# Kernel optimization log

Hardware: AMD Instinct MI355X
Metric: run time of the kernel (lower is better)

## Reference

```python
import jax, jax.numpy as jnp
import numpy as np

SCALE = 0.25  # LoRA alpha / rank


def setup_inputs() -> dict:
    N, K, E, H, D, R = 1024, 2, 16, 1024, 2048, 16
    key = jax.random.key(0)
    ks = jax.random.split(key, 9)
    hidden_states = jax.random.normal(ks[0], (N, D), jnp.float32)
    topk_weights = jax.random.uniform(ks[1], (N, K), jnp.float32)
    topk_weights = topk_weights / topk_weights.sum(-1, keepdims=True)
    topk_ids = jax.random.randint(ks[2], (N, K), 0, E, jnp.int32)
    w_up = jax.random.normal(ks[3], (E, 2 * H, D), jnp.float32) * 0.02
    w_down = jax.random.normal(ks[4], (E, D, H), jnp.float32) * 0.02
    up_a = jax.random.normal(ks[5], (E, R, D), jnp.float32) * 0.02
    up_b = jax.random.normal(ks[6], (E, 2 * H, R), jnp.float32) * 0.02
    down_a = jax.random.normal(ks[7], (E, R, H), jnp.float32) * 0.02
    down_b = jax.random.normal(ks[8], (E, D, R), jnp.float32) * 0.02
    return {
        'hidden_states': hidden_states,
        'topk_weights': topk_weights,
        'topk_ids': topk_ids,
        'w_up': w_up,
        'w_down': w_down,
        'up_a': up_a,
        'up_b': up_b,
        'down_a': down_a,
        'down_b': down_b,
    }


def reference(hidden_states, topk_weights, topk_ids, w_up, w_down, up_a, up_b, down_a, down_b):
    H = w_down.shape[2]  # hidden_size
    # Up projection: dense per-expert GEMM, then gather the selected expert per (token, k).
    up_dense = jnp.einsum('nd,eod->neo', hidden_states, w_up)          # [N, E, 2H]
    up = jnp.take_along_axis(up_dense, topk_ids[:, :, None], axis=1)   # [N, K, 2H]
    # LoRA on up-proj: out[:, k] += (x @ A_e.T @ B_e.T) * scale
    t = jnp.einsum('nd,nkrd->nkr', hidden_states, up_a[topk_ids])      # [N, K, R]
    up = up + SCALE * jnp.einsum('nkr,nkor->nko', t, up_b[topk_ids])   # [N, K, 2H]
    # fused_gelu_and_mul: gelu(first half) * second half (erf gelu)
    act = jax.nn.gelu(up[..., :H], approximate=False) * up[..., H:]    # [N, K, H]
    # Down projection with routed-weight multiply.
    down_dense = jnp.einsum('nkh,edh->nked', act, w_down)              # [N, K, E, D]
    down = jnp.take_along_axis(down_dense, topk_ids[:, :, None, None], axis=2)[:, :, 0, :]  # [N, K, D]
    # LoRA on down-proj (topk_weights applied to lora path too, matching _apply_moe_lora)
    t2 = jnp.einsum('nkh,nkrh->nkr', act, down_a[topk_ids])            # [N, K, R]
    ldown = jnp.einsum('nkr,nkdr->nkd', t2, down_b[topk_ids])          # [N, K, D]
    down = (down + SCALE * ldown) * topk_weights[:, :, None]
    # moe_sum: reduce over top_k
    return down.sum(axis=1)                                            # [N, D]
```

## Files before the change

kernel.cpp:

```cpp
#include <hip/hip_runtime.h>
#include <math.h>

#define N_TOK 1024
#define TOPK  2
#define NEXP  16
#define HID   1024
#define DIM   2048
#define RANK  16
#define NPAIR (N_TOK * TOPK)
#define MOE_SCALE 0.25f
#define MAXTILES 31

typedef __attribute__((ext_vector_type(8))) short short8;
typedef __attribute__((ext_vector_type(4))) float floatx4;

static __device__ __forceinline__ unsigned short f2bf(float f) {
    union { float f; unsigned int u; } v; v.f = f;
    unsigned int u = v.u;
    u += 0x7fffu + ((u >> 16) & 1u);
    return (unsigned short)(u >> 16);
}

static __device__ __forceinline__ short8 cvt8(float4 a, float4 b) {
    short8 o;
    o[0] = (short)f2bf(a.x); o[1] = (short)f2bf(a.y);
    o[2] = (short)f2bf(a.z); o[3] = (short)f2bf(a.w);
    o[4] = (short)f2bf(b.x); o[5] = (short)f2bf(b.y);
    o[6] = (short)f2bf(b.z); o[7] = (short)f2bf(b.w);
    return o;
}

#define XG_T16_STRIDE   (64 * 64 * 8)
#define ACT_T16_STRIDE  (32 * 64 * 8)

__global__ void k_routing(const int* __restrict__ ids,
                          int* __restrict__ offs,
                          int* __restrict__ sorted,
                          int* __restrict__ tlist,
                          int* __restrict__ tcount) {
    __shared__ int s_cnt[NEXP];
    __shared__ int s_off[NEXP + 1];
    int tid = threadIdx.x;
    if (tid < NEXP) s_cnt[tid] = 0;
    __syncthreads();
    for (int p = tid; p < NPAIR; p += blockDim.x) atomicAdd(&s_cnt[ids[p]], 1);
    __syncthreads();
    if (tid == 0) {
        int acc = 0;
        for (int e = 0; e < NEXP; ++e) { s_off[e] = acc; acc += s_cnt[e]; }
        s_off[NEXP] = acc;
        int t = 0;
        for (int e = 0; e < NEXP; ++e) {
            int c = s_off[e + 1] - s_off[e];
            for (int m = 0; m * 128 < c; ++m) tlist[t++] = (e << 8) | m;
        }
        *tcount = t;
    }
    __syncthreads();
    if (tid <= NEXP) offs[tid] = s_off[tid];
    if (tid < NEXP) s_cnt[tid] = s_off[tid];
    __syncthreads();
    for (int p = tid; p < NPAIR; p += blockDim.x) {
        int e = ids[p];
        int slot = atomicAdd(&s_cnt[e], 1);
        sorted[slot] = p;
    }
}

__global__ __launch_bounds__(256) void k_prep(
        const float* __restrict__ x, const int* __restrict__ offs,
        const int* __restrict__ sorted, const int* __restrict__ tlist,
        const int* __restrict__ tcount, unsigned short* __restrict__ xg) {
    int wt = blockIdx.x;
    if (wt >= *tcount) return;
    int code = tlist[wt];
    int e = code >> 8, mt = code & 255;
    int off = offs[e], cnt = offs[e + 1] - off;
    int tid = threadIdx.x, lane = tid & 63, wv = tid >> 6;
    int C = blockIdx.y * 4 + wv;
    int r16 = lane & 15, lq = lane >> 4;
#pragma unroll
    for (int st = 0; st < 8; ++st) {
        int g = mt * 128 + st * 16 + r16; if (g >= cnt) g = cnt - 1;
        int tok = sorted[off + g] >> 1;
        const float* src = x + (size_t)tok * DIM + C * 32 + lq * 8;
        float4 a = *(const float4*)src;
        float4 b = *(const float4*)(src + 4);
        int T16 = wt * 8 + st;
        *(short8*)(xg + (size_t)T16 * XG_T16_STRIDE + (size_t)(C * 64 + lane) * 8)
            = cvt8(a, b);
    }
}

#define LOADB2(t, B, P0, P1) do {                                            \
    const float* _g = (P0) + (size_t)(t) * 64;                               \
    const float* _m = (P1) + (size_t)(t) * 64;                               \
    B[0] = *(const float4*)(_g);      B[1] = *(const float4*)(_g + 4);       \
    B[2] = *(const float4*)(_g + 32); B[3] = *(const float4*)(_g + 36);      \
    B[4] = *(const float4*)(_m);      B[5] = *(const float4*)(_m + 4);       \
    B[6] = *(const float4*)(_m + 32); B[7] = *(const float4*)(_m + 36);      \
} while (0)

#define COMP(t, B, ACC0, ACC1) do {                                          \
    short8 a0[4], a1[4];                                                     \
    _Pragma("unroll") for (int mf = 0; mf < 4; ++mf) {                       \
        a0[mf] = *(const short8*)(ap[mf] + (size_t)(2 * (t)) * 512);         \
        a1[mf] = *(const short8*)(ap[mf] + (size_t)(2 * (t) + 1) * 512);     \
    }                                                                        \
    float4 u0a = *(const float4*)(uq + (size_t)(t) * 64);                    \
    float4 u0b = *(const float4*)(uq + (size_t)(t) * 64 + 4);                \
    float4 u1a = *(const float4*)(uq + (size_t)(t) * 64 + 32);               \
    float4 u1b = *(const float4*)(uq + (size_t)(t) * 64 + 36);               \
    short8 f00 = cvt8(B[0], B[1]), f01 = cvt8(B[2], B[3]);                   \
    short8 f10 = cvt8(B[4], B[5]), f11 = cvt8(B[6], B[7]);                   \
    short8 fu0 = cvt8(u0a, u0b),   fu1 = cvt8(u1a, u1b);                     \
    _Pragma("unroll") for (int mf = 0; mf < 4; ++mf) {                       \
        ACC0[mf] = __builtin_amdgcn_mfma_f32_16x16x32_bf16(a0[mf], f00, ACC0[mf], 0, 0, 0); \
        ACC1[mf] = __builtin_amdgcn_mfma_f32_16x16x32_bf16(a0[mf], f10, ACC1[mf], 0, 0, 0); \
        accT[mf] = __builtin_amdgcn_mfma_f32_16x16x32_bf16(a0[mf], fu0, accT[mf], 0, 0, 0); \
        ACC0[mf] = __builtin_amdgcn_mfma_f32_16x16x32_bf16(a1[mf], f01, ACC0[mf], 0, 0, 0); \
        ACC1[mf] = __builtin_amdgcn_mfma_f32_16x16x32_bf16(a1[mf], f11, ACC1[mf], 0, 0, 0); \
        accT[mf] = __builtin_amdgcn_mfma_f32_16x16x32_bf16(a1[mf], fu1, accT[mf], 0, 0, 0); \
    }                                                                        \
} while (0)

#define G_PIPE(NC, ACC0, ACC1)                                               \
    {                                                                        \
        float4 B0[8], B1[8];                                                 \
        LOADB2(0, B0, bp0, bp1);                                             \
        _Pragma("unroll 1")                                                  \
        for (int t = 0; t + 2 < (NC); t += 2) {                              \
            LOADB2(t + 1, B1, bp0, bp1);                                     \
            COMP(t, B0, ACC0, ACC1);                                         \
            LOADB2(t + 2, B0, bp0, bp1);                                     \
            COMP(t + 1, B1, ACC0, ACC1);                                     \
        }                                                                    \
        LOADB2((NC) - 1, B1, bp0, bp1);                                      \
        COMP((NC) - 2, B0, ACC0, ACC1);                                      \
        COMP((NC) - 1, B1, ACC0, ACC1);                                      \
    }

__global__ __launch_bounds__(256, 2) void k_up(
        const unsigned short* __restrict__ xg, const float* __restrict__ w_up,
        const float* __restrict__ up_a, const float* __restrict__ up_b,
        const int* __restrict__ tlist, const int* __restrict__ tcount,
        unsigned short* __restrict__ actg) {
    int wt = blockIdx.x;
    if (wt >= *tcount) return;
    int code = tlist[wt];
    int e = code >> 8;
    int nt = blockIdx.y;

    int tid = threadIdx.x, lane = tid & 63, wv = tid >> 6;
    int tokg = wv & 1, hg = wv >> 1;
    int lm = lane & 15, lq = lane >> 4;

    const unsigned short* ap[4];
#pragma unroll
    for (int mf = 0; mf < 4; ++mf) {
        int T16 = wt * 8 + tokg * 4 + mf;
        ap[mf] = xg + (size_t)T16 * XG_T16_STRIDE + (size_t)lane * 8;
    }
    int h = nt * 32 + hg * 16 + lm;
    const float* bp0 = w_up + ((size_t)e * 2 * HID + h) * DIM + lq * 8;
    const float* bp1 = w_up + ((size_t)e * 2 * HID + HID + h) * DIM + lq * 8;
    const float* uq  = up_a + ((size_t)e * RANK + lm) * DIM + lq * 8;

    floatx4 zero = {0.f, 0.f, 0.f, 0.f};
    floatx4 accG[4], accM[4], accT[4];
#pragma unroll
    for (int i = 0; i < 4; ++i) { accG[i] = zero; accM[i] = zero; accT[i] = zero; }

    G_PIPE(32, accG, accM);

    __shared__ float t_s[128 * 16];
    if (wv < 2) {
#pragma unroll
        for (int mf = 0; mf < 4; ++mf)
#pragma unroll
            for (int j = 0; j < 4; ++j)
                t_s[(tokg * 64 + mf * 16 + lq * 4 + j) * 16 + lm] = MOE_SCALE * accT[mf][j];
    }
    __syncthreads();

    const float* b1 = up_b + ((size_t)e * 2 * HID + h) * RANK;
    const float* b2 = up_b + ((size_t)e * 2 * HID + HID + h) * RANK;
    float r1[RANK], r2[RANK];
#pragma unroll
    for (int i = 0; i < RANK; ++i) { r1[i] = b1[i]; r2[i] = b2[i]; }
    int C = h >> 5, lsub = 16 * ((h >> 3) & 3), el = h & 7;
#pragma unroll
    for (int mf = 0; mf < 4; ++mf) {
        int T16 = wt * 8 + tokg * 4 + mf;
        unsigned short* dst = actg + (size_t)T16 * ACT_T16_STRIDE + (size_t)C * 512 + el;
#pragma unroll
        for (int r = 0; r < 4; ++r) {
            int rl = tokg * 64 + mf * 16 + lq * 4 + r;
            const float* tv = t_s + rl * 16;
            float s1 = accG[mf][r], s2 = accM[mf][r];
#pragma unroll
            for (int j = 0; j < RANK; ++j) { s1 += tv[j] * r1[j]; s2 += tv[j] * r2[j]; }
            float gl = 0.5f * s1 * (1.f + erff(s1 * 0.70710678118654752f));
            dst[(size_t)(lq * 4 + r + lsub) * 8] = f2bf(gl * s2);
        }
    }
}

__global__ __launch_bounds__(256, 2) void k_down(
        const unsigned short* __restrict__ actg, const float* __restrict__ w_down,
        const float* __restrict__ tw, const float* __restrict__ down_a,
        const float* __restrict__ down_b, const int* __restrict__ offs,
        const int* __restrict__ sorted, const int* __restrict__ tlist,
        const int* __restrict__ tcount, float* __restrict__ out) {
    int wt = blockIdx.x;
    if (wt >= *tcount) return;
    int code = tlist[wt];
    int e = code >> 8, mt = code & 255;
    int nt = blockIdx.y;
    int off = offs[e], cnt = offs[e + 1] - off;

    int tid = threadIdx.x, lane = tid & 63, wv = tid >> 6;
    int tokg = wv & 1, hg = wv >> 1;
    int lm = lane & 15, lq = lane >> 4;

    const unsigned short* ap[4];
#pragma unroll
    for (int mf = 0; mf < 4; ++mf) {
        int T16 = wt * 8 + tokg * 4 + mf;
        ap[mf] = actg + (size_t)T16 * ACT_T16_STRIDE + (size_t)lane * 8;
    }
    int d0 = nt * 64 + hg * 32 + lm;
    const float* bp0 = w_down + ((size_t)e * DIM + d0) * HID + lq * 8;
    const float* bp1 = w_down + ((size_t)e * DIM + d0 + 16) * HID + lq * 8;
    const float* uq  = down_a + ((size_t)e * RANK + lm) * HID + lq * 8;

    floatx4 zero = {0.f, 0.f, 0.f, 0.f};
    floatx4 acc0[4], acc1[4], accT[4];
#pragma unroll
    for (int i = 0; i < 4; ++i) { acc0[i] = zero; acc1[i] = zero; accT[i] = zero; }

    G_PIPE(16, acc0, acc1);

    __shared__ float t_s[128 * 16];
    if (wv < 2) {
#pragma unroll
        for (int mf = 0; mf < 4; ++mf)
#pragma unroll
            for (int j = 0; j < 4; ++j)
                t_s[(tokg * 64 + mf * 16 + lq * 4 + j) * 16 + lm] = MOE_SCALE * accT[mf][j];
    }
    __syncthreads();

    const float* q0 = down_b + ((size_t)e * DIM + d0) * RANK;
    const float* q1 = down_b + ((size_t)e * DIM + d0 + 16) * RANK;
    float rb0[RANK], rb1[RANK];
#pragma unroll
    for (int i = 0; i < RANK; ++i) { rb0[i] = q0[i]; rb1[i] = q1[i]; }
#pragma unroll
    for (int mf = 0; mf < 4; ++mf) {
#pragma unroll
        for (int r = 0; r < 4; ++r) {
            int rl = tokg * 64 + mf * 16 + lq * 4 + r;
            int gg = mt * 128 + rl;
            if (gg < cnt) {
                int pp = sorted[off + gg];
                const float* tv = t_s + rl * 16;
                float v0 = acc0[mf][r], v1 = acc1[mf][r];
#pragma unroll
                for (int j = 0; j < RANK; ++j) { v0 += tv[j] * rb0[j]; v1 += tv[j] * rb1[j]; }
                float w = tw[pp];
                float* op = out + (size_t)(pp >> 1) * DIM;
                atomicAdd(op + d0, v0 * w);
                atomicAdd(op + d0 + 16, v1 * w);
            }
        }
    }
}

extern "C" void kernel_launch(void* const* d_in, const int* in_sizes, int n_in,
                              void* d_out, int out_size, void* d_ws, size_t ws_size,
                              hipStream_t stream) {
    const float* x      = (const float*)d_in[0];
    const float* tw     = (const float*)d_in[1];
    const int*   ids    = (const int*)d_in[2];
    const float* w_up   = (const float*)d_in[3];
    const float* w_down = (const float*)d_in[4];
    const float* up_a   = (const float*)d_in[5];
    const float* up_b   = (const float*)d_in[6];
    const float* down_a = (const float*)d_in[7];
    const float* down_b = (const float*)d_in[8];
    float* out = (float*)d_out;

    char* ws = (char*)d_ws;
    int* offs   = (int*)ws;
    int* tlist  = (int*)(ws + 1024);
    int* tcount = (int*)(ws + 2048);
    int* sorted = (int*)(ws + 4096);
    unsigned short* xg   = (unsigned short*)(ws + 65536);
    unsigned short* actg = (unsigned short*)(ws + 65536 + (size_t)MAXTILES * 8 * XG_T16_STRIDE * 2);

    hipMemsetAsync(d_out, 0, (size_t)out_size * sizeof(float), stream);

    k_routing<<<1, 256, 0, stream>>>(ids, offs, sorted, tlist, tcount);

    dim3 gprep(MAXTILES, 16);
    k_prep<<<gprep, 256, 0, stream>>>(x, offs, sorted, tlist, tcount, xg);

    dim3 gup(MAXTILES, 32);
    k_up<<<gup, 256, 0, stream>>>(xg, w_up, up_a, up_b, tlist, tcount, actg);

    dim3 gdn(MAXTILES, 32);
    k_down<<<gdn, 256, 0, stream>>>(actg, w_down, tw, down_a, down_b, offs, sorted, tlist, tcount, out);
}
```

Before: 728.3 us.

## Split LoRA-A projections into separate kernels and remap block grid for XCD locality

Moves the LoRA A-projection (x·A^T and act·A^T) out of the main up/down GEMM kernels into small dedicated kernels that write per-tile rank vectors to workspace. Previously every one of the 32 N-tile blocks recomputed the same A-projection redundantly; now it is computed once per token tile and loaded into shared memory. The main GEMM pipeline is restructured to prefetch A and B fragments one k-step ahead with fewer MFMAs per step. Blocks are linearised and remapped so consecutive blocks on an XCD share token tiles. The bf16 conversion now uses the HIP intrinsic. The cost is two extra kernel launches and a workspace round trip.

```diff
diff --git a/kernel.cpp b/kernel.cpp
--- a/kernel.cpp
+++ b/kernel.cpp
@@ -1,4 +1,5 @@
 #include <hip/hip_runtime.h>
+#include <hip/hip_bf16.h>
 #include <math.h>
 
 #define N_TOK 1024
@@ -10,15 +11,15 @@
 #define NPAIR (N_TOK * TOPK)
 #define MOE_SCALE 0.25f
 #define MAXTILES 31
+#define NT16 (MAXTILES * 8)
 
 typedef __attribute__((ext_vector_type(8))) short short8;
 typedef __attribute__((ext_vector_type(4))) float floatx4;
 
 static __device__ __forceinline__ unsigned short f2bf(float f) {
-    union { float f; unsigned int u; } v; v.f = f;
-    unsigned int u = v.u;
-    u += 0x7fffu + ((u >> 16) & 1u);
-    return (unsigned short)(u >> 16);
+    union { __hip_bfloat16 b; unsigned short u; } v;
+    v.b = __float2bfloat16(f);
+    return v.u;
 }
 
 static __device__ __forceinline__ short8 cvt8(float4 a, float4 b) {
@@ -92,69 +93,122 @@
     }
 }
 
-#define LOADB2(t, B, P0, P1) do {                                            \
-    const float* _g = (P0) + (size_t)(t) * 64;                               \
-    const float* _m = (P1) + (size_t)(t) * 64;                               \
-    B[0] = *(const float4*)(_g);      B[1] = *(const float4*)(_g + 4);       \
-    B[2] = *(const float4*)(_g + 32); B[3] = *(const float4*)(_g + 36);      \
-    B[4] = *(const float4*)(_m);      B[5] = *(const float4*)(_m + 4);       \
-    B[6] = *(const float4*)(_m + 32); B[7] = *(const float4*)(_m + 36);      \
+__global__ __launch_bounds__(64) void k_tupg(
+        const unsigned short* __restrict__ xg, const float* __restrict__ up_a,
+        const int* __restrict__ tlist, const int* __restrict__ tcount,
+        float* __restrict__ tup) {
+    int T16 = blockIdx.x;
+    if ((T16 >> 3) >= *tcount) return;
+    int e = tlist[T16 >> 3] >> 8;
+    int lane = threadIdx.x, lm = lane & 15, lq = lane >> 4;
+    const unsigned short* ap = xg + (size_t)T16 * XG_T16_STRIDE + (size_t)lane * 8;
+    const float* up = up_a + ((size_t)e * RANK + lm) * DIM + lq * 8;
+    floatx4 zero = {0.f, 0.f, 0.f, 0.f};
+    floatx4 a0 = zero, a1 = zero;
+#pragma unroll 4
+    for (int t = 0; t < 64; t += 2) {
+        short8 f0 = *(const short8*)(ap + (size_t)t * 512);
+        short8 f1 = *(const short8*)(ap + (size_t)(t + 1) * 512);
+        float4 u00 = *(const float4*)(up + t * 32);
+        float4 u01 = *(const float4*)(up + t * 32 + 4);
+        float4 u10 = *(const float4*)(up + (t + 1) * 32);
+        float4 u11 = *(const float4*)(up + (t + 1) * 32 + 4);
+        a0 = __builtin_amdgcn_mfma_f32_16x16x32_bf16(f0, cvt8(u00, u01), a0, 0, 0, 0);
+        a1 = __builtin_amdgcn_mfma_f32_16x16x32_bf16(f1, cvt8(u10, u11), a1, 0, 0, 0);
+    }
+#pragma unroll
+    for (int j = 0; j < 4; ++j)
+        tup[(size_t)T16 * 256 + (lq * 4 + j) * 16 + lm] = MOE_SCALE * (a0[j] + a1[j]);
+}
+
+__global__ __launch_bounds__(64) void k_t2g(
+        const unsigned short* __restrict__ actg, const float* __restrict__ down_a,
+        const int* __restrict__ tlist, const int* __restrict__ tcount,
+        float* __restrict__ t2t) {
+    int T16 = blockIdx.x;
+    if ((T16 >> 3) >= *tcount) return;
+    int e = tlist[T16 >> 3] >> 8;
+    int lane = threadIdx.x, lm = lane & 15, lq = lane >> 4;
+    const unsigned short* ap = actg + (size_t)T16 * ACT_T16_STRIDE + (size_t)lane * 8;
+    const float* da = down_a + ((size_t)e * RANK + lm) * HID + lq * 8;
+    floatx4 zero = {0.f, 0.f, 0.f, 0.f};
+    floatx4 a0 = zero, a1 = zero;
+#pragma unroll 4
+    for (int t = 0; t < 32; t += 2) {
+        short8 f0 = *(const short8*)(ap + (size_t)t * 512);
+        short8 f1 = *(const short8*)(ap + (size_t)(t + 1) * 512);
+        float4 u00 = *(const float4*)(da + t * 32);
+        float4 u01 = *(const float4*)(da + t * 32 + 4);
+        float4 u10 = *(const float4*)(da + (t + 1) * 32);
+        float4 u11 = *(const float4*)(da + (t + 1) * 32 + 4);
+        a0 = __builtin_amdgcn_mfma_f32_16x16x32_bf16(f0, cvt8(u00, u01), a0, 0, 0, 0);
+        a1 = __builtin_amdgcn_mfma_f32_16x16x32_bf16(f1, cvt8(u10, u11), a1, 0, 0, 0);
+    }
+#pragma unroll
+    for (int j = 0; j < 4; ++j)
+        t2t[(size_t)T16 * 256 + (lq * 4 + j) * 16 + lm] = MOE_SCALE * (a0[j] + a1[j]);
+}
+
+#define ISSUE_A(t, AR) do {                                                  \
+    _Pragma("unroll") for (int mf = 0; mf < 4; ++mf)                         \
+        AR[mf] = *(const short8*)(ap[mf] + (size_t)(t) * 512);               \
 } while (0)
 
-#define COMP(t, B, ACC0, ACC1) do {                                          \
-    short8 a0[4], a1[4];                                                     \
+#define ISSUE_B(t, BR) do {                                                  \
+    const float* _g = bpG + (size_t)(t) * 32;                                \
+    const float* _m = bpM + (size_t)(t) * 32;                                \
+    BR[0] = *(const float4*)_g; BR[1] = *(const float4*)(_g + 4);            \
+    BR[2] = *(const float4*)_m; BR[3] = *(const float4*)(_m + 4);            \
+} while (0)
+
+#define CONSUME(AR, BR, ACCX, ACCY) do {                                     \
+    short8 _fx = cvt8(BR[0], BR[1]);                                         \
+    short8 _fy = cvt8(BR[2], BR[3]);                                         \
     _Pragma("unroll") for (int mf = 0; mf < 4; ++mf) {                       \
-        a0[mf] = *(const short8*)(ap[mf] + (size_t)(2 * (t)) * 512);         \
-        a1[mf] = *(const short8*)(ap[mf] + (size_t)(2 * (t) + 1) * 512);     \
-    }                                                                        \
-    float4 u0a = *(const float4*)(uq + (size_t)(t) * 64);                    \
-    float4 u0b = *(const float4*)(uq + (size_t)(t) * 64 + 4);                \
-    float4 u1a = *(const float4*)(uq + (size_t)(t) * 64 + 32);               \
-    float4 u1b = *(const float4*)(uq + (size_t)(t) * 64 + 36);               \
-    short8 f00 = cvt8(B[0], B[1]), f01 = cvt8(B[2], B[3]);                   \
-    short8 f10 = cvt8(B[4], B[5]), f11 = cvt8(B[6], B[7]);                   \
-    short8 fu0 = cvt8(u0a, u0b),   fu1 = cvt8(u1a, u1b);                     \
-    _Pragma("unroll") for (int mf = 0; mf < 4; ++mf) {                       \
-        ACC0[mf] = __builtin_amdgcn_mfma_f32_16x16x32_bf16(a0[mf], f00, ACC0[mf], 0, 0, 0); \
-        ACC1[mf] = __builtin_amdgcn_mfma_f32_16x16x32_bf16(a0[mf], f10, ACC1[mf], 0, 0, 0); \
-        accT[mf] = __builtin_amdgcn_mfma_f32_16x16x32_bf16(a0[mf], fu0, accT[mf], 0, 0, 0); \
-        ACC0[mf] = __builtin_amdgcn_mfma_f32_16x16x32_bf16(a1[mf], f01, ACC0[mf], 0, 0, 0); \
-        ACC1[mf] = __builtin_amdgcn_mfma_f32_16x16x32_bf16(a1[mf], f11, ACC1[mf], 0, 0, 0); \
-        accT[mf] = __builtin_amdgcn_mfma_f32_16x16x32_bf16(a1[mf], fu1, accT[mf], 0, 0, 0); \
+        ACCX[mf] = __builtin_amdgcn_mfma_f32_16x16x32_bf16(AR[mf], _fx, ACCX[mf], 0, 0, 0); \
+        ACCY[mf] = __builtin_amdgcn_mfma_f32_16x16x32_bf16(AR[mf], _fy, ACCY[mf], 0, 0, 0); \
     }                                                                        \
 } while (0)
 
-#define G_PIPE(NC, ACC0, ACC1)                                               \
-    {                                                                        \
-        float4 B0[8], B1[8];                                                 \
-        LOADB2(0, B0, bp0, bp1);                                             \
-        _Pragma("unroll 1")                                                  \
-        for (int t = 0; t + 2 < (NC); t += 2) {                              \
-            LOADB2(t + 1, B1, bp0, bp1);                                     \
-            COMP(t, B0, ACC0, ACC1);                                         \
-            LOADB2(t + 2, B0, bp0, bp1);                                     \
-            COMP(t + 1, B1, ACC0, ACC1);                                     \
-        }                                                                    \
-        LOADB2((NC) - 1, B1, bp0, bp1);                                      \
-        COMP((NC) - 2, B0, ACC0, ACC1);                                      \
-        COMP((NC) - 1, B1, ACC0, ACC1);                                      \
-    }
+#define G_PIPE(NC, ACCX, ACCY) do {                                          \
+    short8 A0[4], A1[4];                                                     \
+    float4 B0[4], B1[4];                                                     \
+    ISSUE_A(0, A0); ISSUE_B(0, B0);                                          \
+    ISSUE_A(1, A1); ISSUE_B(1, B1);                                          \
+    _Pragma("unroll 1")                                                      \
+    for (int t = 0; t < (NC); t += 2) {                                      \
+        CONSUME(A0, B0, ACCX, ACCY);                                         \
+        if (t + 2 < (NC)) { ISSUE_A(t + 2, A0); ISSUE_B(t + 2, B0); }        \
+        CONSUME(A1, B1, ACCX, ACCY);                                         \
+        if (t + 3 < (NC)) { ISSUE_A(t + 3, A1); ISSUE_B(t + 3, B1); }        \
+    }                                                                        \
+} while (0)
+
+#define DECODE_WT_NT()                                                       \
+    int lin = blockIdx.x;                                                    \
+    int glob = (lin & 7) * 124 + (lin >> 3);                                 \
+    int wt = glob >> 5, nt = glob & 31;
 
 __global__ __launch_bounds__(256, 2) void k_up(
         const unsigned short* __restrict__ xg, const float* __restrict__ w_up,
-        const float* __restrict__ up_a, const float* __restrict__ up_b,
+        const float* __restrict__ tup, const float* __restrict__ up_b,
         const int* __restrict__ tlist, const int* __restrict__ tcount,
         unsigned short* __restrict__ actg) {
-    int wt = blockIdx.x;
+    DECODE_WT_NT();
     if (wt >= *tcount) return;
-    int code = tlist[wt];
-    int e = code >> 8;
-    int nt = blockIdx.y;
+    int e = tlist[wt] >> 8;
 
     int tid = threadIdx.x, lane = tid & 63, wv = tid >> 6;
     int tokg = wv & 1, hg = wv >> 1;
     int lm = lane & 15, lq = lane >> 4;
 
+    __shared__ float t_s[128 * 16];
+    {
+        const float* tsrc = tup + (size_t)wt * 2048;
+#pragma unroll
+        for (int j = 0; j < 8; ++j) t_s[tid * 8 + j] = tsrc[tid * 8 + j];
+    }
+
     const unsigned short* ap[4];
 #pragma unroll
     for (int mf = 0; mf < 4; ++mf) {
@@ -162,25 +216,16 @@
         ap[mf] = xg + (size_t)T16 * XG_T16_STRIDE + (size_t)lane * 8;
     }
     int h = nt * 32 + hg * 16 + lm;
-    const float* bp0 = w_up + ((size_t)e * 2 * HID + h) * DIM + lq * 8;
-    const float* bp1 = w_up + ((size_t)e * 2 * HID + HID + h) * DIM + lq * 8;
-    const float* uq  = up_a + ((size_t)e * RANK + lm) * DIM + lq * 8;
+    const float* bpG = w_up + ((size_t)e * 2 * HID + h) * DIM + lq * 8;
+    const float* bpM = w_up + ((size_t)e * 2 * HID + HID + h) * DIM + lq * 8;
 
     floatx4 zero = {0.f, 0.f, 0.f, 0.f};
-    floatx4 accG[4], accM[4], accT[4];
-#pragma unroll
-    for (int i = 0; i < 4; ++i) { accG[i] = zero; accM[i] = zero; accT[i] = zero; }
-
-    G_PIPE(32, accG, accM);
-
-    __shared__ float t_s[128 * 16];
-    if (wv < 2) {
-#pragma unroll
-        for (int mf = 0; mf < 4; ++mf)
-#pragma unroll
-            for (int j = 0; j < 4; ++j)
-                t_s[(tokg * 64 + mf * 16 + lq * 4 + j) * 16 + lm] = MOE_SCALE * accT[mf][j];
-    }
+    floatx4 accG[4], accM[4];
+#pragma unroll
+    for (int i = 0; i < 4; ++i) { accG[i] = zero; accM[i] = zero; }
+
+    G_PIPE(64, accG, accM);
+
     __syncthreads();
 
     const float* b1 = up_b + ((size_t)e * 2 * HID + h) * RANK;
@@ -208,21 +253,27 @@
 
 __global__ __launch_bounds__(256, 2) void k_down(
         const unsigned short* __restrict__ actg, const float* __restrict__ w_down,
-        const float* __restrict__ tw, const float* __restrict__ down_a,
+        const float* __restrict__ tw, const float* __restrict__ t2t,
         const float* __restrict__ down_b, const int* __restrict__ offs,
         const int* __restrict__ sorted, const int* __restrict__ tlist,
         const int* __restrict__ tcount, float* __restrict__ out) {
-    int wt = blockIdx.x;
+    DECODE_WT_NT();
     if (wt >= *tcount) return;
     int code = tlist[wt];
     int e = code >> 8, mt = code & 255;
-    int nt = blockIdx.y;
     int off = offs[e], cnt = offs[e + 1] - off;
 
     int tid = threadIdx.x, lane = tid & 63, wv = tid >> 6;
     int tokg = wv & 1, hg = wv >> 1;
     int lm = lane & 15, lq = lane >> 4;
 
+    __shared__ float t_s[128 * 16];
+    {
+        const float* tsrc = t2t + (size_t)wt * 2048;
+#pragma unroll
+        for (int j = 0; j < 8; ++j) t_s[tid * 8 + j] = tsrc[tid * 8 + j];
+    }
+
     const unsigned short* ap[4];
 #pragma unroll
     for (int mf = 0; mf < 4; ++mf) {
@@ -230,25 +281,16 @@
         ap[mf] = actg + (size_t)T16 * ACT_T16_STRIDE + (size_t)lane * 8;
     }
     int d0 = nt * 64 + hg * 32 + lm;
-    const float* bp0 = w_down + ((size_t)e * DIM + d0) * HID + lq * 8;
-    const float* bp1 = w_down + ((size_t)e * DIM + d0 + 16) * HID + lq * 8;
-    const float* uq  = down_a + ((size_t)e * RANK + lm) * HID + lq * 8;
+    const float* bpG = w_down + ((size_t)e * DIM + d0) * HID + lq * 8;
+    const float* bpM = w_down + ((size_t)e * DIM + d0 + 16) * HID + lq * 8;
 
     floatx4 zero = {0.f, 0.f, 0.f, 0.f};
-    floatx4 acc0[4], acc1[4], accT[4];
-#pragma unroll
-    for (int i = 0; i < 4; ++i) { acc0[i] = zero; acc1[i] = zero; accT[i] = zero; }
-
-    G_PIPE(16, acc0, acc1);
-
-    __shared__ float t_s[128 * 16];
-    if (wv < 2) {
-#pragma unroll
-        for (int mf = 0; mf < 4; ++mf)
-#pragma unroll
-            for (int j = 0; j < 4; ++j)
-                t_s[(tokg * 64 + mf * 16 + lq * 4 + j) * 16 + lm] = MOE_SCALE * accT[mf][j];
-    }
+    floatx4 acc0[4], acc1[4];
+#pragma unroll
+    for (int i = 0; i < 4; ++i) { acc0[i] = zero; acc1[i] = zero; }
+
+    G_PIPE(32, acc0, acc1);
+
     __syncthreads();
 
     const float* q0 = down_b + ((size_t)e * DIM + d0) * RANK;
@@ -292,12 +334,15 @@
     float* out = (float*)d_out;
 
     char* ws = (char*)d_ws;
-    int* offs   = (int*)ws;
-    int* tlist  = (int*)(ws + 1024);
-    int* tcount = (int*)(ws + 2048);
-    int* sorted = (int*)(ws + 4096);
-    unsigned short* xg   = (unsigned short*)(ws + 65536);
-    unsigned short* actg = (unsigned short*)(ws + 65536 + (size_t)MAXTILES * 8 * XG_T16_STRIDE * 2);
+    int*   offs   = (int*)ws;
+    int*   tlist  = (int*)(ws + 1024);
+    int*   tcount = (int*)(ws + 2048);
+    int*   sorted = (int*)(ws + 4096);
+    float* tup    = (float*)(ws + 16384);
+    float* t2t    = (float*)(ws + 16384 + 262144);
+    unsigned short* xg   = (unsigned short*)(ws + 1048576);
+    unsigned short* actg = (unsigned short*)(ws + 1048576
+                              + (size_t)NT16 * XG_T16_STRIDE * 2);
 
     hipMemsetAsync(d_out, 0, (size_t)out_size * sizeof(float), stream);
 
@@ -306,9 +351,12 @@
     dim3 gprep(MAXTILES, 16);
     k_prep<<<gprep, 256, 0, stream>>>(x, offs, sorted, tlist, tcount, xg);
 
-    dim3 gup(MAXTILES, 32);
-    k_up<<<gup, 256, 0, stream>>>(xg, w_up, up_a, up_b, tlist, tcount, actg);
-
-    dim3 gdn(MAXTILES, 32);
-    k_down<<<gdn, 256, 0, stream>>>(actg, w_down, tw, down_a, down_b, offs, sorted, tlist, tcount, out);
-}
+    k_tupg<<<NT16, 64, 0, stream>>>(xg, up_a, tlist, tcount, tup);
+
+    k_up<<<MAXTILES * 32, 256, 0, stream>>>(xg, w_up, tup, up_b, tlist, tcount, actg);
+
+    k_t2g<<<NT16, 64, 0, stream>>>(actg, down_a, tlist, tcount, t2t);
+
+    k_down<<<MAXTILES * 32, 256, 0, stream>>>(actg, w_down, tw, t2t, down_b,
+                                              offs, sorted, tlist, tcount, out);
+}
```

After: 663.3 us. 8.9% less time.
